# Kernel tuning notes

Measured on AMD Instinct MI355X. Metric: run time of the kernel, lower is better.

## Reference

```python
import jax, jax.numpy as jnp
import numpy as np

N = 50000
E = 640000
R = 8


def setup_inputs() -> dict:
    key = jax.random.key(0)
    ks = jax.random.split(key, 12)
    in_c, hid_c, out_c = 128, 128, 64
    s1 = 1.0 / np.sqrt(in_c)
    s2 = 1.0 / np.sqrt(hid_c)
    s3 = 1.0 / np.sqrt(out_c)
    return {
        "x": jax.random.normal(ks[0], (N, in_c), dtype=jnp.float32),
        "edge_index": jax.random.randint(ks[1], (2, E), 0, N),
        "edge_type": jax.random.randint(ks[2], (E,), 0, R),
        # layer 1: per-relation weights, root weight, bias
        "W1": jax.random.uniform(ks[3], (R, in_c, hid_c), minval=-s1, maxval=s1, dtype=jnp.float32),
        "root1": jax.random.uniform(ks[4], (in_c, hid_c), minval=-s1, maxval=s1, dtype=jnp.float32),
        "b1": jnp.zeros((hid_c,), dtype=jnp.float32),
        # layer 2
        "W2": jax.random.uniform(ks[5], (R, hid_c, out_c), minval=-s2, maxval=s2, dtype=jnp.float32),
        "root2": jax.random.uniform(ks[6], (hid_c, out_c), minval=-s2, maxval=s2, dtype=jnp.float32),
        "b2": jnp.zeros((out_c,), dtype=jnp.float32),
        # classifier
        "Wc": jax.random.uniform(ks[7], (out_c, 2), minval=-s3, maxval=s3, dtype=jnp.float32),
        "bc": jnp.zeros((2,), dtype=jnp.float32),
    }


def _rgcn_layer(x, edge_index, edge_type, W, root, b):
    # PyG RGCNConv with aggr='mean': per relation r, mean-aggregate source
    # features over edges of type r into destinations, then apply W_r.
    # out = sum_r mean_agg_r(x) @ W_r + x @ root + b
    src, dst = edge_index[0], edge_index[1]
    msgs = x[src]  # [E, Fin] gather
    seg = edge_type * N + dst  # combined (relation, dst) segment id
    sums = jax.ops.segment_sum(msgs, seg, num_segments=R * N)  # [R*N, Fin]
    cnt = jax.ops.segment_sum(jnp.ones((msgs.shape[0],), x.dtype), seg, num_segments=R * N)
    mean = sums / jnp.maximum(cnt, 1.0)[:, None]  # zero-degree -> 0
    mean = mean.reshape(R, N, x.shape[1])  # [R, N, Fin]
    out = jnp.einsum("rnf,rfo->no", mean, W) + x @ root + b
    return out


def reference(x, edge_index, edge_type, W1, root1, b1, W2, root2, b2, Wc, bc):
    h = jax.nn.relu(_rgcn_layer(x, edge_index, edge_type, W1, root1, b1))
    # dropout (p=0.3) is identity in eval mode
    h = jax.nn.relu(_rgcn_layer(h, edge_index, edge_type, W2, root2, b2))
    logits = h @ Wc + bc  # [N, 2]
    return logits
```

## Files before the change

kernel.cpp:

```cpp
#include <hip/hip_runtime.h>

#define NN 50000
#define EE 640000
#define RR 8
#define CAP 64

typedef __bf16 bf16x8 __attribute__((ext_vector_type(8)));
typedef float  f32x4  __attribute__((ext_vector_type(4)));
typedef const __attribute__((address_space(1))) unsigned int* gas_p;
typedef __attribute__((address_space(3))) unsigned int* las_p;

__device__ __forceinline__ unsigned short f2b(float f) {
  unsigned int u = __float_as_uint(f);
  u += 0x7fffu + ((u >> 16) & 1u);
  return (unsigned short)(u >> 16);
}
__device__ __forceinline__ float b2f(unsigned short h) {
  return __uint_as_float(((unsigned int)h) << 16);
}

__device__ __forceinline__ float edge_scale(unsigned int e, int lane, int deg) {
  unsigned long long valid = __ballot(lane < deg);
  unsigned long long m0 = __ballot((e >> 16) & 1u);
  unsigned long long m1 = __ballot((e >> 17) & 1u);
  unsigned long long m2 = __ballot((e >> 18) & 1u);
  unsigned long long mm = ((e >> 16) & 1u ? m0 : ~m0);
  mm &= ((e >> 17) & 1u ? m1 : ~m1);
  mm &= ((e >> 18) & 1u ? m2 : ~m2);
  mm &= valid;
  return (lane < deg) ? __builtin_amdgcn_rcpf((float)__popcll(mm)) : 0.f;
}

#define CONV_N 1600000
#define B1_N (1152 * 128)
#define B2_N (640 * 128)
__global__ void k_prologue(const float* __restrict__ x, unsigned short* __restrict__ xb,
                           const float* __restrict__ W1, const float* __restrict__ root1,
                           unsigned short* __restrict__ B1T,
                           const float* __restrict__ W2, const float* __restrict__ root2,
                           unsigned short* __restrict__ B2T,
                           const int* __restrict__ srcI, const int* __restrict__ dstI,
                           const int* __restrict__ typ,
                           int* __restrict__ cursor, unsigned int* __restrict__ entries) {
  int t = blockIdx.x * 256 + threadIdx.x;
  if (t < CONV_N) {
    float4 v = reinterpret_cast<const float4*>(x)[t];
    ushort4 o = make_ushort4(f2b(v.x), f2b(v.y), f2b(v.z), f2b(v.w));
    reinterpret_cast<ushort4*>(xb)[t] = o;
    return;
  }
  t -= CONV_N;
  if (t < B1_N) {
    int j = t >> 7, k = t & 127;
    float v = (j < 1024) ? W1[((j >> 7) << 14) + (k << 7) + (j & 127)]
                         : root1[(k << 7) + (j - 1024)];
    B1T[t] = f2b(v);
    return;
  }
  t -= B1_N;
  if (t < B2_N) {
    int j = t >> 7, k = t & 127;
    float v = 0.0f;
    if (j < 512)      v = W2[((j >> 6) << 13) + (k << 6) + (j & 63)];
    else if (j < 576) v = root2[(k << 6) + (j - 512)];
    B2T[t] = f2b(v);
    return;
  }
  t -= B2_N;
  if (t < EE) {
    int d = dstI[t], r = typ[t];
    int pos = atomicAdd(&cursor[d], 1);
    if (pos < CAP)
      entries[d * CAP + pos] = (unsigned int)srcI[t] | ((unsigned int)r << 16);
  }
}

__global__ __launch_bounds__(256, 3) void k_gemm(
    const unsigned short* __restrict__ A, const unsigned short* __restrict__ BT,
    unsigned short* __restrict__ Y, float* __restrict__ rootOut,
    const float* __restrict__ bias, int M, int nsplit, int nroot, int nsub) {
  __shared__ __align__(16) unsigned short Bs[2][64 * 128];
  const int tid = threadIdx.x;
  const int m0 = blockIdx.x * 128;
  const int n0g = blockIdx.y * nsub * 64;
  const int lane = tid & 63;
  const int wave = tid >> 6;
  const int wm = (wave >> 1) << 6;
  const int wn = (wave & 1) << 5;
  const int l15 = lane & 15;
  const int quad = lane >> 4;

  {
    const unsigned short* Gb = BT + (size_t)n0g * 128;
#pragma unroll
    for (int c = 0; c < 4; ++c) {
      int L = tid + c * 256;
      int r = L >> 4, c16 = L & 15;
      int j = c16 ^ (r & 15);
      __builtin_amdgcn_global_load_lds(
          (gas_p)(const void*)(Gb + (size_t)r * 128 + j * 8),
          (las_p)(void*)(Bs[0] + r * 128 + c16 * 8), 16, 0, 0);
    }
  }

  bf16x8 af[4][4];
#pragma unroll
  for (int kk = 0; kk < 4; ++kk)
#pragma unroll
    for (int i = 0; i < 4; ++i)
      af[kk][i] = *reinterpret_cast<const bf16x8*>(
          A + (size_t)(m0 + wm + i * 16 + l15) * 128 + (kk * 4 + quad) * 8);

  __syncthreads();

  const int tr = lane >> 2;
  const int tc = lane & 3;
  const int sl0 = ((tc & 1) << 1) * 16 + tr;
  const int sl1 = sl0 + 16;
  const bool thi = (tc & 2) != 0;

  int buf = 0;
  for (int s = 0; s < nsub; ++s) {
    if (s + 1 < nsub) {
      const unsigned short* Gb = BT + (size_t)(n0g + (s + 1) * 64) * 128;
      unsigned short* Lb = Bs[buf ^ 1];
#pragma unroll
      for (int c = 0; c < 4; ++c) {
        int L = tid + c * 256;
        int r = L >> 4, c16 = L & 15;
        int j = c16 ^ (r & 15);
        __builtin_amdgcn_global_load_lds(
            (gas_p)(const void*)(Gb + (size_t)r * 128 + j * 8),
            (las_p)(void*)(Lb + r * 128 + c16 * 8), 16, 0, 0);
      }
    }

    f32x4 acc[4][2] = {};
    const unsigned short* Bc = Bs[buf];
#pragma unroll
    for (int kk = 0; kk < 4; ++kk) {
      const int sw = ((kk * 4 + quad) ^ l15) * 8;
      bf16x8 bfr[2];
#pragma unroll
      for (int j = 0; j < 2; ++j)
        bfr[j] = *reinterpret_cast<const bf16x8*>(&Bc[(wn + j * 16 + l15) * 128 + sw]);
#pragma unroll
      for (int i = 0; i < 4; ++i)
#pragma unroll
        for (int j = 0; j < 2; ++j)
          acc[i][j] = __builtin_amdgcn_mfma_f32_16x16x32_bf16(bfr[j], af[kk][i], acc[i][j], 0, 0, 0);
    }
    __syncthreads();

    const int scol = n0g + s * 64;
    if (scol >= nsplit) {
#pragma unroll
      for (int i = 0; i < 4; ++i) {
        const int m = wm + i * 16 + l15;
        if (m0 + m >= M) continue;
#pragma unroll
        for (int j = 0; j < 2; ++j) {
          const int col = scol + wn + j * 16 + quad * 4 - nsplit;
          if (col < nroot) {
            float4 b4 = *reinterpret_cast<const float4*>(&bias[col]);
            float4 v = make_float4(acc[i][j][0] + b4.x, acc[i][j][1] + b4.y,
                                   acc[i][j][2] + b4.z, acc[i][j][3] + b4.w);
            *reinterpret_cast<float4*>(&rootOut[(size_t)(m0 + m) * nroot + col]) = v;
          }
        }
      }
    } else {
#pragma unroll
      for (int i = 0; i < 4; ++i) {
        uint2 pk0, pk1;
        pk0.x = (unsigned int)f2b(acc[i][0][0]) | ((unsigned int)f2b(acc[i][0][1]) << 16);
        pk0.y = (unsigned int)f2b(acc[i][0][2]) | ((unsigned int)f2b(acc[i][0][3]) << 16);
        pk1.x = (unsigned int)f2b(acc[i][1][0]) | ((unsigned int)f2b(acc[i][1][1]) << 16);
        pk1.y = (unsigned int)f2b(acc[i][1][2]) | ((unsigned int)f2b(acc[i][1][3]) << 16);
        unsigned int a0x = __shfl(pk0.x, sl0, 64), a0y = __shfl(pk0.y, sl0, 64);
        unsigned int a1x = __shfl(pk1.x, sl0, 64), a1y = __shfl(pk1.y, sl0, 64);
        unsigned int b0x = __shfl(pk0.x, sl1, 64), b0y = __shfl(pk0.y, sl1, 64);
        unsigned int b1x = __shfl(pk1.x, sl1, 64), b1y = __shfl(pk1.y, sl1, 64);
        uint4 o;
        o.x = thi ? a1x : a0x;
        o.y = thi ? a1y : a0y;
        o.z = thi ? b1x : b0x;
        o.w = thi ? b1y : b0y;
        const int m = wm + i * 16 + tr;
        if (m0 + m < M)
          *reinterpret_cast<uint4*>(&Y[(size_t)(m0 + m) * nsplit + scol + wn + tc * 8]) = o;
      }
    }
    buf ^= 1;
  }
}

#define ACC8(pk, s)                                          \
  a[0] += b2f((unsigned short)pk.x) * s;                     \
  a[1] += __uint_as_float(pk.x & 0xffff0000u) * s;           \
  a[2] += b2f((unsigned short)pk.y) * s;                     \
  a[3] += __uint_as_float(pk.y & 0xffff0000u) * s;           \
  a[4] += b2f((unsigned short)pk.z) * s;                     \
  a[5] += __uint_as_float(pk.z & 0xffff0000u) * s;           \
  a[6] += b2f((unsigned short)pk.w) * s;                     \
  a[7] += __uint_as_float(pk.w & 0xffff0000u) * s;

__global__ void k_agg1(const unsigned int* __restrict__ entries,
                       const int* __restrict__ cursor,
                       const unsigned short* __restrict__ y,
                       const float* __restrict__ hpre,
                       unsigned int* __restrict__ hbf) {
  const int d = blockIdx.x * 4 + (threadIdx.x >> 6);
  const int lane = threadIdx.x & 63;
  int deg = cursor[d];
  if (deg > CAP) deg = CAP;
  unsigned int e = (lane < deg) ? entries[d * CAP + lane] : 0u;
  float sc = edge_scale(e, lane, deg);

  const int g = lane >> 4;
  const int l16 = lane & 15;

  float4 h0, h1;
  if (g == 0) {
    const float4* hp = reinterpret_cast<const float4*>(hpre) + (size_t)d * 32 + l16 * 2;
    h0 = hp[0];
    h1 = hp[1];
  }

  float a[8] = {};
  const int T = (deg + 15) >> 4;
  for (int t = 0; t < T; ++t) {
    const int base = t * 16 + g;
    unsigned int e0 = __shfl(e, base, 64);       float s0 = __shfl(sc, base, 64);
    unsigned int e1 = __shfl(e, base + 4, 64);   float s1 = __shfl(sc, base + 4, 64);
    unsigned int e2 = __shfl(e, base + 8, 64);   float s2 = __shfl(sc, base + 8, 64);
    unsigned int e3 = __shfl(e, base + 12, 64);  float s3 = __shfl(sc, base + 12, 64);
    uint4 p0 = *reinterpret_cast<const uint4*>(
        y + (((size_t)(e0 & 0xffffu)) << 10) + (((e0 >> 16) & 7u) << 7) + (l16 << 3));
    uint4 p1 = *reinterpret_cast<const uint4*>(
        y + (((size_t)(e1 & 0xffffu)) << 10) + (((e1 >> 16) & 7u) << 7) + (l16 << 3));
    uint4 p2 = *reinterpret_cast<const uint4*>(
        y + (((size_t)(e2 & 0xffffu)) << 10) + (((e2 >> 16) & 7u) << 7) + (l16 << 3));
    uint4 p3 = *reinterpret_cast<const uint4*>(
        y + (((size_t)(e3 & 0xffffu)) << 10) + (((e3 >> 16) & 7u) << 7) + (l16 << 3));
    ACC8(p0, s0);
    ACC8(p1, s1);
    ACC8(p2, s2);
    ACC8(p3, s3);
  }
#pragma unroll
  for (int j = 0; j < 8; ++j) {
    a[j] += __shfl_xor(a[j], 16, 64);
    a[j] += __shfl_xor(a[j], 32, 64);
  }
  if (g == 0) {
    float v0 = fmaxf(a[0] + h0.x, 0.f), v1 = fmaxf(a[1] + h0.y, 0.f);
    float v2 = fmaxf(a[2] + h0.z, 0.f), v3 = fmaxf(a[3] + h0.w, 0.f);
    float v4 = fmaxf(a[4] + h1.x, 0.f), v5 = fmaxf(a[5] + h1.y, 0.f);
    float v6 = fmaxf(a[6] + h1.z, 0.f), v7 = fmaxf(a[7] + h1.w, 0.f);
    uint4 o;
    o.x = (unsigned int)f2b(v0) | ((unsigned int)f2b(v1) << 16);
    o.y = (unsigned int)f2b(v2) | ((unsigned int)f2b(v3) << 16);
    o.z = (unsigned int)f2b(v4) | ((unsigned int)f2b(v5) << 16);
    o.w = (unsigned int)f2b(v6) | ((unsigned int)f2b(v7) << 16);
    reinterpret_cast<uint4*>(hbf)[(size_t)d * 16 + l16] = o;
  }
}

__global__ void k_agg2(const unsigned int* __restrict__ entries,
                       const int* __restrict__ cursor,
                       const unsigned short* __restrict__ y,
                       const float* __restrict__ hpre,
                       const float* __restrict__ Wc, const float* __restrict__ bc,
                       float* __restrict__ out) {
  const int d = blockIdx.x * 4 + (threadIdx.x >> 6);
  const int lane = threadIdx.x & 63;
  int deg = cursor[d];
  if (deg > CAP) deg = CAP;
  unsigned int e = (lane < deg) ? entries[d * CAP + lane] : 0u;
  float sc = edge_scale(e, lane, deg);

  const int g = lane >> 3;
  const int l8 = lane & 7;

  const float4* hp = reinterpret_cast<const float4*>(hpre) + (size_t)d * 16 + l8 * 2;
  float4 h0 = hp[0];
  float4 h1 = hp[1];

  float a[8] = {};
  const int T = (deg + 31) >> 5;
  for (int t = 0; t < T; ++t) {
    const int base = t * 32 + g;
    unsigned int e0 = __shfl(e, base, 64);       float s0 = __shfl(sc, base, 64);
    unsigned int e1 = __shfl(e, base + 8, 64);   float s1 = __shfl(sc, base + 8, 64);
    unsigned int e2 = __shfl(e, base + 16, 64);  float s2 = __shfl(sc, base + 16, 64);
    unsigned int e3 = __shfl(e, base + 24, 64);  float s3 = __shfl(sc, base + 24, 64);
    uint4 p0 = *reinterpret_cast<const uint4*>(
        y + (((size_t)(e0 & 0xffffu)) << 9) + (((e0 >> 16) & 7u) << 6) + (l8 << 3));
    uint4 p1 = *reinterpret_cast<const uint4*>(
        y + (((size_t)(e1 & 0xffffu)) << 9) + (((e1 >> 16) & 7u) << 6) + (l8 << 3));
    uint4 p2 = *reinterpret_cast<const uint4*>(
        y + (((size_t)(e2 & 0xffffu)) << 9) + (((e2 >> 16) & 7u) << 6) + (l8 << 3));
    uint4 p3 = *reinterpret_cast<const uint4*>(
        y + (((size_t)(e3 & 0xffffu)) << 9) + (((e3 >> 16) & 7u) << 6) + (l8 << 3));
    ACC8(p0, s0);
    ACC8(p1, s1);
    ACC8(p2, s2);
    ACC8(p3, s3);
  }
#pragma unroll
  for (int j = 0; j < 8; ++j) {
    a[j] += __shfl_xor(a[j], 8, 64);
    a[j] += __shfl_xor(a[j], 16, 64);
    a[j] += __shfl_xor(a[j], 32, 64);
  }
  float v0 = fmaxf(a[0] + h0.x, 0.f), v1 = fmaxf(a[1] + h0.y, 0.f);
  float v2 = fmaxf(a[2] + h0.z, 0.f), v3 = fmaxf(a[3] + h0.w, 0.f);
  float v4 = fmaxf(a[4] + h1.x, 0.f), v5 = fmaxf(a[5] + h1.y, 0.f);
  float v6 = fmaxf(a[6] + h1.z, 0.f), v7 = fmaxf(a[7] + h1.w, 0.f);
  const float4* wc4 = reinterpret_cast<const float4*>(Wc) + l8 * 4;
  float4 w0 = wc4[0], w1 = wc4[1], w2 = wc4[2], w3 = wc4[3];
  float p0 = v0 * w0.x + v1 * w0.z + v2 * w1.x + v3 * w1.z
           + v4 * w2.x + v5 * w2.z + v6 * w3.x + v7 * w3.z;
  float p1 = v0 * w0.y + v1 * w0.w + v2 * w1.y + v3 * w1.w
           + v4 * w2.y + v5 * w2.w + v6 * w3.y + v7 * w3.w;
  p0 += __shfl_xor(p0, 1, 64); p1 += __shfl_xor(p1, 1, 64);
  p0 += __shfl_xor(p0, 2, 64); p1 += __shfl_xor(p1, 2, 64);
  p0 += __shfl_xor(p0, 4, 64); p1 += __shfl_xor(p1, 4, 64);
  if (lane == 0) {
    out[d * 2 + 0] = p0 + bc[0];
    out[d * 2 + 1] = p1 + bc[1];
  }
}

extern "C" void kernel_launch(void* const* d_in, const int* in_sizes, int n_in,
                              void* d_out, int out_size, void* d_ws, size_t ws_size,
                              hipStream_t stream) {
  const float* x     = (const float*)d_in[0];
  const int*   ei    = (const int*)d_in[1];
  const int*   et    = (const int*)d_in[2];
  const float* W1    = (const float*)d_in[3];
  const float* root1 = (const float*)d_in[4];
  const float* b1    = (const float*)d_in[5];
  const float* W2    = (const float*)d_in[6];
  const float* root2 = (const float*)d_in[7];
  const float* b2    = (const float*)d_in[8];
  const float* Wc    = (const float*)d_in[9];
  const float* bc    = (const float*)d_in[10];
  const int* srcI = ei;
  const int* dstI = ei + EE;

  char* ws = (char*)d_ws;
  unsigned short* xb      = (unsigned short*)(ws);
  unsigned int*   hbf     = (unsigned int*)(ws);
  unsigned short* B1T     = (unsigned short*)(ws + 12800000);
  unsigned short* B2T     = (unsigned short*)(ws + 13094912);
  int*            cursor  = (int*)(ws + 13258752);
  unsigned int*   entries = (unsigned int*)(ws + 13458752);
  float*          hpre    = (float*)(ws + 26258752);
  unsigned short* y1      = (unsigned short*)(ws + 51858752);
  unsigned short* y2      = y1;

  hipMemsetAsync(cursor, 0, 200000, stream);

  const int PRO_N = CONV_N + B1_N + B2_N + EE;
  k_prologue<<<(PRO_N + 255) / 256, 256, 0, stream>>>(x, xb, W1, root1, B1T,
                                                      W2, root2, B2T,
                                                      srcI, dstI, et, cursor, entries);

  k_gemm<<<dim3(391, 3), 256, 0, stream>>>(xb, B1T, y1, hpre, b1, NN, 1024, 128, 6);
  k_agg1<<<NN / 4, 256, 0, stream>>>(entries, cursor, y1, hpre, hbf);

  k_gemm<<<dim3(391, 2), 256, 0, stream>>>((const unsigned short*)hbf, B2T, y2, hpre, b2,
                                           NN, 512, 64, 5);
  k_agg2<<<NN / 4, 256, 0, stream>>>(entries, cursor, y2, hpre, Wc, bc, (float*)d_out);
}
```

Baseline: 267.6 us.

## Fuse aggregate-then-transform per layer into one kernel with LDS-staged means

The separate GEMM and aggregation kernels are replaced with one fused kernel per layer. For each relation it gathers and mean-aggregates neighbour features into LDS, then multiplies by that relation's weight with MFMA, adds the root term, and finishes with bias/ReLU (and the classifier in layer 2). This removes the large intermediate Y buffers and the extra launches. In exchange, 128-row blocks run 8 serial relation passes, each re-reading the edge list and gathering features, with only 391 blocks. The cursor array is padded to a 16-int stride and CAP drops from 64 to 48, which risks silently dropping edges for high-degree nodes.

After: 965.9 us. 3.61x slower.

```diff
diff --git a/kernel.cpp b/kernel.cpp
--- a/kernel.cpp
+++ b/kernel.cpp
@@ -3,12 +3,11 @@
 #define NN 50000
 #define EE 640000
 #define RR 8
-#define CAP 64
+#define CAP 48
+#define CSTRIDE 16
 
 typedef __bf16 bf16x8 __attribute__((ext_vector_type(8)));
 typedef float  f32x4  __attribute__((ext_vector_type(4)));
-typedef const __attribute__((address_space(1))) unsigned int* gas_p;
-typedef __attribute__((address_space(3))) unsigned int* las_p;
 
 __device__ __forceinline__ unsigned short f2b(float f) {
   unsigned int u = __float_as_uint(f);
@@ -17,18 +16,6 @@
 }
 __device__ __forceinline__ float b2f(unsigned short h) {
   return __uint_as_float(((unsigned int)h) << 16);
-}
-
-__device__ __forceinline__ float edge_scale(unsigned int e, int lane, int deg) {
-  unsigned long long valid = __ballot(lane < deg);
-  unsigned long long m0 = __ballot((e >> 16) & 1u);
-  unsigned long long m1 = __ballot((e >> 17) & 1u);
-  unsigned long long m2 = __ballot((e >> 18) & 1u);
-  unsigned long long mm = ((e >> 16) & 1u ? m0 : ~m0);
-  mm &= ((e >> 17) & 1u ? m1 : ~m1);
-  mm &= ((e >> 18) & 1u ? m2 : ~m2);
-  mm &= valid;
-  return (lane < deg) ? __builtin_amdgcn_rcpf((float)__popcll(mm)) : 0.f;
 }
 
 #define CONV_N 1600000
@@ -69,114 +56,148 @@
   t -= B2_N;
   if (t < EE) {
     int d = dstI[t], r = typ[t];
-    int pos = atomicAdd(&cursor[d], 1);
+    int pos = atomicAdd(&cursor[d * CSTRIDE], 1);
     if (pos < CAP)
-      entries[d * CAP + pos] = (unsigned int)srcI[t] | ((unsigned int)r << 16);
-  }
-}
-
-__global__ __launch_bounds__(256, 3) void k_gemm(
-    const unsigned short* __restrict__ A, const unsigned short* __restrict__ BT,
-    unsigned short* __restrict__ Y, float* __restrict__ rootOut,
-    const float* __restrict__ bias, int M, int nsplit, int nroot, int nsub) {
-  __shared__ __align__(16) unsigned short Bs[2][64 * 128];
+      entries[(size_t)d * CAP + pos] = (unsigned int)srcI[t] | ((unsigned int)r << 16);
+  }
+}
+
+template <int NOUT, bool CLS>
+__global__ __launch_bounds__(256, 3) void k_fused(
+    const unsigned short* __restrict__ X,
+    const unsigned short* __restrict__ BT,
+    const unsigned int* __restrict__ entries,
+    const int* __restrict__ cursor,
+    const float* __restrict__ bias,
+    unsigned short* __restrict__ H,
+    const float* __restrict__ Wc, const float* __restrict__ bc,
+    float* __restrict__ out) {
+  __shared__ __align__(16) unsigned char smem[CLS ? 34816 : 32768];
+  unsigned short* Ms = reinterpret_cast<unsigned short*>(smem);
   const int tid = threadIdx.x;
-  const int m0 = blockIdx.x * 128;
-  const int n0g = blockIdx.y * nsub * 64;
   const int lane = tid & 63;
   const int wave = tid >> 6;
+  const int d0 = blockIdx.x * 128;
+  constexpr int JW = NOUT / 32;
   const int wm = (wave >> 1) << 6;
-  const int wn = (wave & 1) << 5;
+  const int wn = (wave & 1) * (NOUT / 2);
   const int l15 = lane & 15;
   const int quad = lane >> 4;
-
-  {
-    const unsigned short* Gb = BT + (size_t)n0g * 128;
-#pragma unroll
-    for (int c = 0; c < 4; ++c) {
-      int L = tid + c * 256;
-      int r = L >> 4, c16 = L & 15;
-      int j = c16 ^ (r & 15);
-      __builtin_amdgcn_global_load_lds(
-          (gas_p)(const void*)(Gb + (size_t)r * 128 + j * 8),
-          (las_p)(void*)(Bs[0] + r * 128 + c16 * 8), 16, 0, 0);
-    }
-  }
-
-  bf16x8 af[4][4];
-#pragma unroll
-  for (int kk = 0; kk < 4; ++kk)
-#pragma unroll
-    for (int i = 0; i < 4; ++i)
-      af[kk][i] = *reinterpret_cast<const bf16x8*>(
-          A + (size_t)(m0 + wm + i * 16 + l15) * 128 + (kk * 4 + quad) * 8);
-
-  __syncthreads();
-
-  const int tr = lane >> 2;
-  const int tc = lane & 3;
-  const int sl0 = ((tc & 1) << 1) * 16 + tr;
-  const int sl1 = sl0 + 16;
-  const bool thi = (tc & 2) != 0;
-
-  int buf = 0;
-  for (int s = 0; s < nsub; ++s) {
-    if (s + 1 < nsub) {
-      const unsigned short* Gb = BT + (size_t)(n0g + (s + 1) * 64) * 128;
-      unsigned short* Lb = Bs[buf ^ 1];
-#pragma unroll
-      for (int c = 0; c < 4; ++c) {
-        int L = tid + c * 256;
-        int r = L >> 4, c16 = L & 15;
-        int j = c16 ^ (r & 15);
-        __builtin_amdgcn_global_load_lds(
-            (gas_p)(const void*)(Gb + (size_t)r * 128 + j * 8),
-            (las_p)(void*)(Lb + r * 128 + c16 * 8), 16, 0, 0);
-      }
-    }
-
-    f32x4 acc[4][2] = {};
-    const unsigned short* Bc = Bs[buf];
-#pragma unroll
-    for (int kk = 0; kk < 4; ++kk) {
-      const int sw = ((kk * 4 + quad) ^ l15) * 8;
-      bf16x8 bfr[2];
-#pragma unroll
-      for (int j = 0; j < 2; ++j)
-        bfr[j] = *reinterpret_cast<const bf16x8*>(&Bc[(wn + j * 16 + l15) * 128 + sw]);
-#pragma unroll
-      for (int i = 0; i < 4; ++i)
-#pragma unroll
-        for (int j = 0; j < 2; ++j)
-          acc[i][j] = __builtin_amdgcn_mfma_f32_16x16x32_bf16(bfr[j], af[kk][i], acc[i][j], 0, 0, 0);
-    }
-    __syncthreads();
-
-    const int scol = n0g + s * 64;
-    if (scol >= nsplit) {
-#pragma unroll
-      for (int i = 0; i < 4; ++i) {
-        const int m = wm + i * 16 + l15;
-        if (m0 + m >= M) continue;
-#pragma unroll
-        for (int j = 0; j < 2; ++j) {
-          const int col = scol + wn + j * 16 + quad * 4 - nsplit;
-          if (col < nroot) {
-            float4 b4 = *reinterpret_cast<const float4*>(&bias[col]);
-            float4 v = make_float4(acc[i][j][0] + b4.x, acc[i][j][1] + b4.y,
-                                   acc[i][j][2] + b4.z, acc[i][j][3] + b4.w);
-            *reinterpret_cast<float4*>(&rootOut[(size_t)(m0 + m) * nroot + col]) = v;
+  const int g = quad;
+  const int l16 = l15;
+
+  f32x4 acc[4][JW] = {};
+
+  for (int r = 0; r < 8; ++r) {
+    for (int t = 0; t < 32; ++t) {
+      const int dl = (wave << 5) + t;
+      const int d = d0 + dl;
+      int deg = (d < NN) ? cursor[d * CSTRIDE] : 0;
+      if (deg > CAP) deg = CAP;
+      unsigned int e = (lane < deg) ? entries[(size_t)d * CAP + lane] : 0u;
+      const bool match = (lane < deg) && (((e >> 16) & 7u) == (unsigned)r);
+      unsigned long long bm = __ballot(match);
+      int cnt = __popcll(bm);
+      float sc = match ? __builtin_amdgcn_rcpf((float)cnt) : 0.f;
+      float a[8] = {};
+      const int T = (deg + 15) >> 4;
+      for (int tt = 0; tt < T; ++tt) {
+#pragma unroll
+        for (int q = 0; q < 4; ++q) {
+          const int slot = tt * 16 + q * 4 + g;
+          unsigned int eq = __shfl(e, slot, 64);
+          float sq = __shfl(sc, slot, 64);
+          if (sq != 0.f) {
+            uint4 p = *reinterpret_cast<const uint4*>(
+                X + (((size_t)(eq & 0xffffu)) << 7) + (l16 << 3));
+            a[0] += b2f((unsigned short)p.x) * sq;
+            a[1] += __uint_as_float(p.x & 0xffff0000u) * sq;
+            a[2] += b2f((unsigned short)p.y) * sq;
+            a[3] += __uint_as_float(p.y & 0xffff0000u) * sq;
+            a[4] += b2f((unsigned short)p.z) * sq;
+            a[5] += __uint_as_float(p.z & 0xffff0000u) * sq;
+            a[6] += b2f((unsigned short)p.w) * sq;
+            a[7] += __uint_as_float(p.w & 0xffff0000u) * sq;
           }
         }
       }
-    } else {
+#pragma unroll
+      for (int j2 = 0; j2 < 8; ++j2) {
+        a[j2] += __shfl_xor(a[j2], 16, 64);
+        a[j2] += __shfl_xor(a[j2], 32, 64);
+      }
+      if (g == 0) {
+        uint4 o4;
+        o4.x = (unsigned int)f2b(a[0]) | ((unsigned int)f2b(a[1]) << 16);
+        o4.y = (unsigned int)f2b(a[2]) | ((unsigned int)f2b(a[3]) << 16);
+        o4.z = (unsigned int)f2b(a[4]) | ((unsigned int)f2b(a[5]) << 16);
+        o4.w = (unsigned int)f2b(a[6]) | ((unsigned int)f2b(a[7]) << 16);
+        *reinterpret_cast<uint4*>(&Ms[dl * 128 + ((l16 ^ (dl & 15)) << 3)]) = o4;
+      }
+    }
+    __syncthreads();
+#pragma unroll
+    for (int kk = 0; kk < 4; ++kk) {
+      const int sw = ((kk * 4 + quad) ^ l15) << 3;
+      bf16x8 af[4], bfr[JW];
+#pragma unroll
+      for (int i = 0; i < 4; ++i)
+        af[i] = *reinterpret_cast<const bf16x8*>(&Ms[(wm + i * 16 + l15) * 128 + sw]);
+#pragma unroll
+      for (int j = 0; j < JW; ++j)
+        bfr[j] = *reinterpret_cast<const bf16x8*>(
+            BT + (size_t)(r * NOUT + wn + j * 16 + l15) * 128 + (kk * 4 + quad) * 8);
+#pragma unroll
+      for (int i = 0; i < 4; ++i)
+#pragma unroll
+        for (int j = 0; j < JW; ++j)
+          acc[i][j] = __builtin_amdgcn_mfma_f32_16x16x32_bf16(bfr[j], af[i], acc[i][j], 0, 0, 0);
+    }
+    __syncthreads();
+  }
+
+#pragma unroll
+  for (int kk = 0; kk < 4; ++kk) {
+    bf16x8 af[4], bfr[JW];
+#pragma unroll
+    for (int i = 0; i < 4; ++i) {
+      int rA = d0 + wm + i * 16 + l15;
+      if (rA > NN - 1) rA = NN - 1;
+      af[i] = *reinterpret_cast<const bf16x8*>(X + (size_t)rA * 128 + (kk * 4 + quad) * 8);
+    }
+#pragma unroll
+    for (int j = 0; j < JW; ++j)
+      bfr[j] = *reinterpret_cast<const bf16x8*>(
+          BT + (size_t)(8 * NOUT + wn + j * 16 + l15) * 128 + (kk * 4 + quad) * 8);
+#pragma unroll
+    for (int i = 0; i < 4; ++i)
+#pragma unroll
+      for (int j = 0; j < JW; ++j)
+        acc[i][j] = __builtin_amdgcn_mfma_f32_16x16x32_bf16(bfr[j], af[i], acc[i][j], 0, 0, 0);
+  }
+
+  if constexpr (!CLS) {
+    const int tr = lane >> 2;
+    const int tc = lane & 3;
+    const int sl0 = ((tc & 1) << 1) * 16 + tr;
+    const int sl1 = sl0 + 16;
+    const bool thi = (tc & 2) != 0;
+#pragma unroll
+    for (int grp = 0; grp < 2; ++grp) {
 #pragma unroll
       for (int i = 0; i < 4; ++i) {
+        float4 b0 = *reinterpret_cast<const float4*>(&bias[wn + grp * 32 + quad * 4]);
+        float4 b1_ = *reinterpret_cast<const float4*>(&bias[wn + grp * 32 + 16 + quad * 4]);
+        f32x4 v0 = acc[i][grp * 2 + 0], v1 = acc[i][grp * 2 + 1];
+        float e0 = fmaxf(v0[0] + b0.x, 0.f), e1 = fmaxf(v0[1] + b0.y, 0.f);
+        float e2 = fmaxf(v0[2] + b0.z, 0.f), e3 = fmaxf(v0[3] + b0.w, 0.f);
+        float f0 = fmaxf(v1[0] + b1_.x, 0.f), f1 = fmaxf(v1[1] + b1_.y, 0.f);
+        float f2 = fmaxf(v1[2] + b1_.z, 0.f), f3 = fmaxf(v1[3] + b1_.w, 0.f);
         uint2 pk0, pk1;
-        pk0.x = (unsigned int)f2b(acc[i][0][0]) | ((unsigned int)f2b(acc[i][0][1]) << 16);
-        pk0.y = (unsigned int)f2b(acc[i][0][2]) | ((unsigned int)f2b(acc[i][0][3]) << 16);
-        pk1.x = (unsigned int)f2b(acc[i][1][0]) | ((unsigned int)f2b(acc[i][1][1]) << 16);
-        pk1.y = (unsigned int)f2b(acc[i][1][2]) | ((unsigned int)f2b(acc[i][1][3]) << 16);
+        pk0.x = (unsigned int)f2b(e0) | ((unsigned int)f2b(e1) << 16);
+        pk0.y = (unsigned int)f2b(e2) | ((unsigned int)f2b(e3) << 16);
+        pk1.x = (unsigned int)f2b(f0) | ((unsigned int)f2b(f1) << 16);
+        pk1.y = (unsigned int)f2b(f2) | ((unsigned int)f2b(f3) << 16);
         unsigned int a0x = __shfl(pk0.x, sl0, 64), a0y = __shfl(pk0.y, sl0, 64);
         unsigned int a1x = __shfl(pk1.x, sl0, 64), a1y = __shfl(pk1.y, sl0, 64);
         unsigned int b0x = __shfl(pk0.x, sl1, 64), b0y = __shfl(pk0.y, sl1, 64);
@@ -187,149 +208,41 @@
         o.z = thi ? b1x : b0x;
         o.w = thi ? b1y : b0y;
         const int m = wm + i * 16 + tr;
-        if (m0 + m < M)
-          *reinterpret_cast<uint4*>(&Y[(size_t)(m0 + m) * nsplit + scol + wn + tc * 8]) = o;
-      }
-    }
-    buf ^= 1;
-  }
-}
-
-#define ACC8(pk, s)                                          \
-  a[0] += b2f((unsigned short)pk.x) * s;                     \
-  a[1] += __uint_as_float(pk.x & 0xffff0000u) * s;           \
-  a[2] += b2f((unsigned short)pk.y) * s;                     \
-  a[3] += __uint_as_float(pk.y & 0xffff0000u) * s;           \
-  a[4] += b2f((unsigned short)pk.z) * s;                     \
-  a[5] += __uint_as_float(pk.z & 0xffff0000u) * s;           \
-  a[6] += b2f((unsigned short)pk.w) * s;                     \
-  a[7] += __uint_as_float(pk.w & 0xffff0000u) * s;
-
-__global__ void k_agg1(const unsigned int* __restrict__ entries,
-                       const int* __restrict__ cursor,
-                       const unsigned short* __restrict__ y,
-                       const float* __restrict__ hpre,
-                       unsigned int* __restrict__ hbf) {
-  const int d = blockIdx.x * 4 + (threadIdx.x >> 6);
-  const int lane = threadIdx.x & 63;
-  int deg = cursor[d];
-  if (deg > CAP) deg = CAP;
-  unsigned int e = (lane < deg) ? entries[d * CAP + lane] : 0u;
-  float sc = edge_scale(e, lane, deg);
-
-  const int g = lane >> 4;
-  const int l16 = lane & 15;
-
-  float4 h0, h1;
-  if (g == 0) {
-    const float4* hp = reinterpret_cast<const float4*>(hpre) + (size_t)d * 32 + l16 * 2;
-    h0 = hp[0];
-    h1 = hp[1];
-  }
-
-  float a[8] = {};
-  const int T = (deg + 15) >> 4;
-  for (int t = 0; t < T; ++t) {
-    const int base = t * 16 + g;
-    unsigned int e0 = __shfl(e, base, 64);       float s0 = __shfl(sc, base, 64);
-    unsigned int e1 = __shfl(e, base + 4, 64);   float s1 = __shfl(sc, base + 4, 64);
-    unsigned int e2 = __shfl(e, base + 8, 64);   float s2 = __shfl(sc, base + 8, 64);
-    unsigned int e3 = __shfl(e, base + 12, 64);  float s3 = __shfl(sc, base + 12, 64);
-    uint4 p0 = *reinterpret_cast<const uint4*>(
-        y + (((size_t)(e0 & 0xffffu)) << 10) + (((e0 >> 16) & 7u) << 7) + (l16 << 3));
-    uint4 p1 = *reinterpret_cast<const uint4*>(
-        y + (((size_t)(e1 & 0xffffu)) << 10) + (((e1 >> 16) & 7u) << 7) + (l16 << 3));
-    uint4 p2 = *reinterpret_cast<const uint4*>(
-        y + (((size_t)(e2 & 0xffffu)) << 10) + (((e2 >> 16) & 7u) << 7) + (l16 << 3));
-    uint4 p3 = *reinterpret_cast<const uint4*>(
-        y + (((size_t)(e3 & 0xffffu)) << 10) + (((e3 >> 16) & 7u) << 7) + (l16 << 3));
-    ACC8(p0, s0);
-    ACC8(p1, s1);
-    ACC8(p2, s2);
-    ACC8(p3, s3);
-  }
-#pragma unroll
-  for (int j = 0; j < 8; ++j) {
-    a[j] += __shfl_xor(a[j], 16, 64);
-    a[j] += __shfl_xor(a[j], 32, 64);
-  }
-  if (g == 0) {
-    float v0 = fmaxf(a[0] + h0.x, 0.f), v1 = fmaxf(a[1] + h0.y, 0.f);
-    float v2 = fmaxf(a[2] + h0.z, 0.f), v3 = fmaxf(a[3] + h0.w, 0.f);
-    float v4 = fmaxf(a[4] + h1.x, 0.f), v5 = fmaxf(a[5] + h1.y, 0.f);
-    float v6 = fmaxf(a[6] + h1.z, 0.f), v7 = fmaxf(a[7] + h1.w, 0.f);
-    uint4 o;
-    o.x = (unsigned int)f2b(v0) | ((unsigned int)f2b(v1) << 16);
-    o.y = (unsigned int)f2b(v2) | ((unsigned int)f2b(v3) << 16);
-    o.z = (unsigned int)f2b(v4) | ((unsigned int)f2b(v5) << 16);
-    o.w = (unsigned int)f2b(v6) | ((unsigned int)f2b(v7) << 16);
-    reinterpret_cast<uint4*>(hbf)[(size_t)d * 16 + l16] = o;
-  }
-}
-
-__global__ void k_agg2(const unsigned int* __restrict__ entries,
-                       const int* __restrict__ cursor,
-                       const unsigned short* __restrict__ y,
-                       const float* __restrict__ hpre,
-                       const float* __restrict__ Wc, const float* __restrict__ bc,
-                       float* __restrict__ out) {
-  const int d = blockIdx.x * 4 + (threadIdx.x >> 6);
-  const int lane = threadIdx.x & 63;
-  int deg = cursor[d];
-  if (deg > CAP) deg = CAP;
-  unsigned int e = (lane < deg) ? entries[d * CAP + lane] : 0u;
-  float sc = edge_scale(e, lane, deg);
-
-  const int g = lane >> 3;
-  const int l8 = lane & 7;
-
-  const float4* hp = reinterpret_cast<const float4*>(hpre) + (size_t)d * 16 + l8 * 2;
-  float4 h0 = hp[0];
-  float4 h1 = hp[1];
-
-  float a[8] = {};
-  const int T = (deg + 31) >> 5;
-  for (int t = 0; t < T; ++t) {
-    const int base = t * 32 + g;
-    unsigned int e0 = __shfl(e, base, 64);       float s0 = __shfl(sc, base, 64);
-    unsigned int e1 = __shfl(e, base + 8, 64);   float s1 = __shfl(sc, base + 8, 64);
-    unsigned int e2 = __shfl(e, base + 16, 64);  float s2 = __shfl(sc, base + 16, 64);
-    unsigned int e3 = __shfl(e, base + 24, 64);  float s3 = __shfl(sc, base + 24, 64);
-    uint4 p0 = *reinterpret_cast<const uint4*>(
-        y + (((size_t)(e0 & 0xffffu)) << 9) + (((e0 >> 16) & 7u) << 6) + (l8 << 3));
-    uint4 p1 = *reinterpret_cast<const uint4*>(
-        y + (((size_t)(e1 & 0xffffu)) << 9) + (((e1 >> 16) & 7u) << 6) + (l8 << 3));
-    uint4 p2 = *reinterpret_cast<const uint4*>(
-        y + (((size_t)(e2 & 0xffffu)) << 9) + (((e2 >> 16) & 7u) << 6) + (l8 << 3));
-    uint4 p3 = *reinterpret_cast<const uint4*>(
-        y + (((size_t)(e3 & 0xffffu)) << 9) + (((e3 >> 16) & 7u) << 6) + (l8 << 3));
-    ACC8(p0, s0);
-    ACC8(p1, s1);
-    ACC8(p2, s2);
-    ACC8(p3, s3);
-  }
-#pragma unroll
-  for (int j = 0; j < 8; ++j) {
-    a[j] += __shfl_xor(a[j], 8, 64);
-    a[j] += __shfl_xor(a[j], 16, 64);
-    a[j] += __shfl_xor(a[j], 32, 64);
-  }
-  float v0 = fmaxf(a[0] + h0.x, 0.f), v1 = fmaxf(a[1] + h0.y, 0.f);
-  float v2 = fmaxf(a[2] + h0.z, 0.f), v3 = fmaxf(a[3] + h0.w, 0.f);
-  float v4 = fmaxf(a[4] + h1.x, 0.f), v5 = fmaxf(a[5] + h1.y, 0.f);
-  float v6 = fmaxf(a[6] + h1.z, 0.f), v7 = fmaxf(a[7] + h1.w, 0.f);
-  const float4* wc4 = reinterpret_cast<const float4*>(Wc) + l8 * 4;
-  float4 w0 = wc4[0], w1 = wc4[1], w2 = wc4[2], w3 = wc4[3];
-  float p0 = v0 * w0.x + v1 * w0.z + v2 * w1.x + v3 * w1.z
-           + v4 * w2.x + v5 * w2.z + v6 * w3.x + v7 * w3.z;
-  float p1 = v0 * w0.y + v1 * w0.w + v2 * w1.y + v3 * w1.w
-           + v4 * w2.y + v5 * w2.w + v6 * w3.y + v7 * w3.w;
-  p0 += __shfl_xor(p0, 1, 64); p1 += __shfl_xor(p1, 1, 64);
-  p0 += __shfl_xor(p0, 2, 64); p1 += __shfl_xor(p1, 2, 64);
-  p0 += __shfl_xor(p0, 4, 64); p1 += __shfl_xor(p1, 4, 64);
-  if (lane == 0) {
-    out[d * 2 + 0] = p0 + bc[0];
-    out[d * 2 + 1] = p1 + bc[1];
+        if (d0 + m < NN)
+          *reinterpret_cast<uint4*>(&H[(size_t)(d0 + m) * 128 + wn + grp * 32 + tc * 8]) = o;
+      }
+    }
+  } else {
+    float* hs = reinterpret_cast<float*>(smem);
+#pragma unroll
+    for (int i = 0; i < 4; ++i) {
+      const int row = wm + i * 16 + l15;
+#pragma unroll
+      for (int j = 0; j < JW; ++j) {
+        const int col = wn + j * 16 + quad * 4;
+        float4 b4 = *reinterpret_cast<const float4*>(&bias[col]);
+        float4 v = make_float4(fmaxf(acc[i][j][0] + b4.x, 0.f),
+                               fmaxf(acc[i][j][1] + b4.y, 0.f),
+                               fmaxf(acc[i][j][2] + b4.z, 0.f),
+                               fmaxf(acc[i][j][3] + b4.w, 0.f));
+        *reinterpret_cast<float4*>(&hs[row * 68 + col]) = v;
+      }
+    }
+    __syncthreads();
+    if (tid < 128) {
+      const int dl = tid;
+      float p0 = 0.f, p1 = 0.f;
+      for (int o = 0; o < 64; ++o) {
+        float h = hs[dl * 68 + o];
+        p0 += h * Wc[o * 2 + 0];
+        p1 += h * Wc[o * 2 + 1];
+      }
+      const int d = d0 + dl;
+      if (d < NN) {
+        out[d * 2 + 0] = p0 + bc[0];
+        out[d * 2 + 1] = p1 + bc[1];
+      }
+    }
   }
 }
 
@@ -352,26 +265,22 @@
 
   char* ws = (char*)d_ws;
   unsigned short* xb      = (unsigned short*)(ws);
-  unsigned int*   hbf     = (unsigned int*)(ws);
   unsigned short* B1T     = (unsigned short*)(ws + 12800000);
   unsigned short* B2T     = (unsigned short*)(ws + 13094912);
   int*            cursor  = (int*)(ws + 13258752);
-  unsigned int*   entries = (unsigned int*)(ws + 13458752);
-  float*          hpre    = (float*)(ws + 26258752);
-  unsigned short* y1      = (unsigned short*)(ws + 51858752);
-  unsigned short* y2      = y1;
-
-  hipMemsetAsync(cursor, 0, 200000, stream);
+  unsigned int*   entries = (unsigned int*)(ws + 16458752);
+  unsigned short* h1      = (unsigned short*)(ws + 26058752);
+
+  hipMemsetAsync(cursor, 0, 3200000, stream);
 
   const int PRO_N = CONV_N + B1_N + B2_N + EE;
   k_prologue<<<(PRO_N + 255) / 256, 256, 0, stream>>>(x, xb, W1, root1, B1T,
                                                       W2, root2, B2T,
                                                       srcI, dstI, et, cursor, entries);
 
-  k_gemm<<<dim3(391, 3), 256, 0, stream>>>(xb, B1T, y1, hpre, b1, NN, 1024, 128, 6);
-  k_agg1<<<NN / 4, 256, 0, stream>>>(entries, cursor, y1, hpre, hbf);
-
-  k_gemm<<<dim3(391, 2), 256, 0, stream>>>((const unsigned short*)hbf, B2T, y2, hpre, b2,
-                                           NN, 512, 64, 5);
-  k_agg2<<<NN / 4, 256, 0, stream>>>(entries, cursor, y2, hpre, Wc, bc, (float*)d_out);
-}
+  k_fused<128, false><<<391, 256, 0, stream>>>(xb, B1T, entries, cursor, b1,
+                                               h1, nullptr, nullptr, nullptr);
+
+  k_fused<64, true><<<391, 256, 0, stream>>>(h1, B2T, entries, cursor, b2,
+                                             nullptr, Wc, bc, (float*)d_out);
+}
```
